# Kernel optimization log

Measured on AMD Instinct MI355X. Metric: run time of the kernel, lower is better.

Reference implementation:

```python
import jax, jax.numpy as jnp
import numpy as np

D_MODEL = 1024
NHEAD = 16
HEAD_DIM = D_MODEL // NHEAD
EPS = 1e-8


def setup_inputs() -> dict:
    key = jax.random.key(0)
    ks = jax.random.split(key, 10)
    B, T = 2, 2048
    s = 1.0 / np.sqrt(D_MODEL)
    return {
        "query": jax.random.normal(ks[0], (B, T, D_MODEL), jnp.float32),
        "key": jax.random.normal(ks[1], (B, T, D_MODEL), jnp.float32),
        "value": jax.random.normal(ks[2], (B, T, D_MODEL), jnp.float32),
        "frac": jax.random.uniform(ks[3], (B, T), jnp.float32),
        "Wq": jax.random.normal(ks[4], (D_MODEL, D_MODEL), jnp.float32) * s,
        "bq": jnp.zeros((D_MODEL,), jnp.float32),
        "Wk": jax.random.normal(ks[5], (D_MODEL, D_MODEL), jnp.float32) * s,
        "bk": jnp.zeros((D_MODEL,), jnp.float32),
        "Wv": jax.random.normal(ks[6], (D_MODEL, D_MODEL), jnp.float32) * s,
        "bv": jnp.zeros((D_MODEL,), jnp.float32),
        "attn_bias": jax.random.normal(ks[7], (HEAD_DIM,), jnp.float32) * 0.02,
        "Wo": jax.random.normal(ks[8], (D_MODEL, D_MODEL), jnp.float32) * s,
        "bo": jnpp if False else jnp.zeros((D_MODEL,), jnp.float32),
    }


def reference(query, key, value, frac, Wq, bq, Wk, bk, Wv, bv, attn_bias, Wo, bo):
    B, T, _ = query.shape
    H, Dh = NHEAD, HEAD_DIM
    scale = Dh ** -0.5

    # torch Linear: x @ W.T + b
    Q = (query @ Wq.T + bq).reshape(B, T, H, Dh).transpose(0, 2, 1, 3)  # [B,H,T,Dh]
    K = (key @ Wk.T + bk).reshape(B, T, H, Dh).transpose(0, 2, 1, 3)
    V = (value @ Wv.T + bv).reshape(B, T, H, Dh).transpose(0, 2, 1, 3)

    # factor_ij = (frac_j - frac_i) / (frac_i*frac_j + eps), shape [B,T,T]
    fi = frac[:, :, None]
    fj = frac[:, None, :]
    factor = (fj - fi) / (fi * fj + EPS)

    # sum_d (Q_i*K_j + attn_bias*factor)_d == QK^T + sum(attn_bias)*factor
    bias_sum = jnp.sum(attn_bias)
    logits = jnp.einsum('bhid,bhjd->bhij', Q, K) + bias_sum * factor[:, None, :, :]
    logits = logits * scale

    probs = jax.nn.softmax(logits, axis=-1)  # dropout p=0.0 (eval)
    out = jnp.einsum('bhij,bhjd->bhid', probs, V)  # [B,H,T,Dh]
    out = out.transpose(0, 2, 1, 3).reshape(B, T, H * Dh)
    return out @ Wo.T + bo
```

## Files before the change

### kernel.cpp

```cpp
#include <hip/hip_runtime.h>

typedef short s16x8 __attribute__((ext_vector_type(8)));
typedef float f32x4 __attribute__((ext_vector_type(4)));
typedef float f32x16 __attribute__((ext_vector_type(16)));
typedef unsigned int u32x2 __attribute__((ext_vector_type(2)));
typedef unsigned int u32x4 __attribute__((ext_vector_type(4)));
typedef unsigned short u16;
typedef unsigned int u32;

#define D_MODEL 1024
#define NHEAD   16
#define HD      64
#define TSEQ    2048
#define NB      2
#define MROWS   4096
#define NSPLIT  2
#define NTILES  (TSEQ / 64 / NSPLIT)

#define LOG2E 1.4426950408889634f
#define QSCALE (0.125f * LOG2E)

__device__ __forceinline__ u16 f2bf(float f) {
  unsigned u = __builtin_bit_cast(unsigned, f);
  u += 0x7fffu + ((u >> 16) & 1u);
  return (u16)(u >> 16);
}

__device__ __forceinline__ float bf2f(u16 x) {
  return __builtin_bit_cast(float, (u32)x << 16);
}

__device__ __forceinline__ u32 cvtpk(float lo, float hi) {
  u32 r;
  asm("v_cvt_pk_bf16_f32 %0, %1, %2" : "=v"(r) : "v"(lo), "v"(hi));
  return r;
}

__device__ __forceinline__ float exp2fast(float x) {
#if __has_builtin(__builtin_amdgcn_exp2f)
  return __builtin_amdgcn_exp2f(x);
#else
  return exp2f(x);
#endif
}

__device__ __forceinline__ float rcpfast(float x) {
#if __has_builtin(__builtin_amdgcn_rcpf)
  return __builtin_amdgcn_rcpf(x);
#else
  return 1.f / x;
#endif
}

__device__ __forceinline__ void gload16(const void* g, void* l) {
  __builtin_amdgcn_global_load_lds((const __attribute__((address_space(1))) void*)g,
                                   (__attribute__((address_space(3))) void*)l,
                                   16, 0, 0);
}

__global__ void cvt_all(const float* __restrict__ q, const float* __restrict__ k,
                        const float* __restrict__ v, const float* __restrict__ wq,
                        const float* __restrict__ wk, const float* __restrict__ wv,
                        const float* __restrict__ wo, const float* __restrict__ ab,
                        u16* qb, u16* kb, u16* vb, u16* wqb, u16* wkb, u16* wvb, u16* wob,
                        float* bsum) {
  if (blockIdx.x == 16384) {
    if (threadIdx.x < 64) {
      float s = ab[threadIdx.x];
#pragma unroll
      for (int m = 32; m >= 1; m >>= 1) s += __shfl_xor(s, m);
      if (threadIdx.x == 0) bsum[0] = s * 0.125f * LOG2E;
    }
    return;
  }
  int i = blockIdx.x * 256 + threadIdx.x;
  const float* src; u16* dst; int off;
  if (i < 3 * 1048576) {
    int t = i >> 20; off = i & 1048575;
    src = (t == 0) ? q : (t == 1) ? k : v;
    dst = (t == 0) ? qb : (t == 1) ? kb : vb;
  } else {
    int j = i - 3 * 1048576;
    int t = j >> 18; off = j & 262143;
    src = (t == 0) ? wq : (t == 1) ? wk : (t == 2) ? wv : wo;
    dst = (t == 0) ? wqb : (t == 1) ? wkb : (t == 2) ? wvb : wob;
  }
  float4 x = ((const float4*)src)[off];
  ushort4 o;
  o.x = f2bf(x.x); o.y = f2bf(x.y); o.z = f2bf(x.z); o.w = f2bf(x.w);
  ((ushort4*)dst)[off] = o;
}

template <int BM, int BN, int WN, int MODE>
__device__ __forceinline__ void gemm_core(const u16* __restrict__ A, const u16* __restrict__ Bt,
                                          const float* __restrict__ bias, void* __restrict__ out,
                                          float oscale, u16* lds) {
  constexpr int K = 1024, N = 1024;
  constexpr int WM = 4 / WN;
  constexpr int WTM = BM / WM, WTN = BN / WN;
  constexpr int MR = WTM / 16, NR = WTN / 16;
  constexpr int ASZ = BM * 32, BSZ = BN * 32;
  constexpr int AISS = ASZ / 2048, BISS = BSZ / 2048;
  u16* lA = lds;
  u16* lB = lds + 2 * ASZ;

  const int tid = threadIdx.x;
  const int wid = tid >> 6, lane = tid & 63;
  const int l15 = lane & 15, lgp = lane >> 4;
  const int wr = wid / WN, wc = wid % WN;
  const int m0 = blockIdx.y * BM, n0 = blockIdx.x * BN;

  const u16* gA[AISS];
  const u16* gB[BISS];
#pragma unroll
  for (int i = 0; i < AISS; ++i) {
    int tp = i * 256 + tid, row = tp % BM, kc = tp / BM;
    gA[i] = A + (size_t)(m0 + row) * K + kc * 8;
  }
#pragma unroll
  for (int i = 0; i < BISS; ++i) {
    int tp = i * 256 + tid, row = tp % BN, kc = tp / BN;
    gB[i] = Bt + (size_t)(n0 + row) * K + kc * 8;
  }

  f32x4 acc[MR][NR];
#pragma unroll
  for (int m = 0; m < MR; ++m)
#pragma unroll
    for (int n = 0; n < NR; ++n) acc[m][n] = (f32x4){0.f, 0.f, 0.f, 0.f};

  auto stage = [&](int buf, int k0) {
#pragma unroll
    for (int i = 0; i < AISS; ++i)
      gload16(gA[i] + k0, lA + buf * ASZ + (i * 256 + tid) * 8);
#pragma unroll
    for (int i = 0; i < BISS; ++i)
      gload16(gB[i] + k0, lB + buf * BSZ + (i * 256 + tid) * 8);
  };

  int cur = 0;
  stage(0, 0);
  __syncthreads();
  for (int k0 = 0; k0 < K; k0 += 32) {
    if (k0 + 32 < K) stage(cur ^ 1, k0 + 32);
    const u16* a = lA + cur * ASZ;
    const u16* b = lB + cur * BSZ;
    s16x8 af[MR], bf[NR];
#pragma unroll
    for (int m = 0; m < MR; ++m)
      af[m] = *(const s16x8*)(a + lgp * BM * 8 + (wr * WTM + m * 16 + l15) * 8);
#pragma unroll
    for (int n = 0; n < NR; ++n)
      bf[n] = *(const s16x8*)(b + lgp * BN * 8 + (wc * WTN + n * 16 + l15) * 8);
    __builtin_amdgcn_s_setprio(1);
#pragma unroll
    for (int m = 0; m < MR; ++m)
#pragma unroll
      for (int n = 0; n < NR; ++n) {
        if (MODE == 1)
          acc[m][n] = __builtin_amdgcn_mfma_f32_16x16x32_bf16(bf[n], af[m], acc[m][n], 0, 0, 0);
        else
          acc[m][n] = __builtin_amdgcn_mfma_f32_16x16x32_bf16(af[m], bf[n], acc[m][n], 0, 0, 0);
      }
    __builtin_amdgcn_s_setprio(0);
    __syncthreads();
    cur ^= 1;
  }

  if (MODE == 1) {
    float4 bvv4[NR];
#pragma unroll
    for (int n = 0; n < NR; ++n)
      bvv4[n] = *(const float4*)(bias + n0 + wc * WTN + n * 16 + lgp * 4);
#pragma unroll
    for (int m = 0; m < MR; ++m) {
      int m_abs = m0 + wr * WTM + m * 16 + l15;
      int bb = m_abs >> 11, t = m_abs & 2047;
#pragma unroll
      for (int n = 0; n < NR; ++n) {
#pragma unroll
        for (int r = 0; r < 4; ++r) {
          int n_abs = n0 + wc * WTN + n * 16 + lgp * 4 + r;
          int h = n_abs >> 6, d = n_abs & 63;
          float vv = (acc[m][n][r] + ((const float*)&bvv4[n])[r]) * oscale;
          ((u16*)out)[(((size_t)((bb * NHEAD + h) * HD + d)) << 11) + t] = f2bf(vv);
        }
      }
    }
  } else {
    float bvv[NR];
#pragma unroll
    for (int n = 0; n < NR; ++n) bvv[n] = bias[n0 + wc * WTN + n * 16 + l15];
#pragma unroll
    for (int m = 0; m < MR; ++m) {
      int rowb = m0 + wr * WTM + m * 16 + lgp * 4;
#pragma unroll
      for (int n = 0; n < NR; ++n) {
        int col = n0 + wc * WTN + n * 16 + l15;
#pragma unroll
        for (int r = 0; r < 4; ++r) {
          int row = rowb + r;
          float vv = (acc[m][n][r] + bvv[n]) * oscale;
          if (MODE == 2) {
            ((float*)out)[(size_t)row * N + col] = vv;
          } else {
            int b = row >> 11, t = row & 2047;
            int h = col >> 6, d = col & 63;
            ((u16*)out)[(((size_t)(b * NHEAD + h) * TSEQ + t) << 6) + d] = f2bf(vv);
          }
        }
      }
    }
  }
}

__global__ __launch_bounds__(256) void gemm_qkv(const u16* __restrict__ qb, const u16* __restrict__ kb,
                                                const u16* __restrict__ vb,
                                                const u16* __restrict__ Wqb, const u16* __restrict__ Wkb,
                                                const u16* __restrict__ Wvb,
                                                const float* __restrict__ bq, const float* __restrict__ bk,
                                                const float* __restrict__ bv,
                                                u16* Qp, u16* Kp, u16* Vtp) {
  __shared__ __align__(16) u16 lds[2 * 128 * 32 * 2];
  int z = blockIdx.z;
  if (z == 0)
    gemm_core<128, 128, 2, 0>(qb, Wqb, bq, Qp, QSCALE, lds);
  else if (z == 1)
    gemm_core<128, 128, 2, 0>(kb, Wkb, bk, Kp, 1.0f, lds);
  else
    gemm_core<128, 128, 2, 1>(vb, Wvb, bv, Vtp, 1.0f, lds);
}

__global__ __launch_bounds__(256) void gemm_out(const u16* __restrict__ A, const u16* __restrict__ Bt,
                                                const float* __restrict__ bias, float* __restrict__ out) {
  __shared__ __align__(16) u16 lds[2 * 64 * 32 + 2 * 128 * 32];
  gemm_core<64, 128, 4, 2>(A, Bt, bias, out, 1.0f, lds);
}

__global__ __launch_bounds__(256, 4) void attn_kernel(const u16* __restrict__ Qp,
                                                      const u16* __restrict__ Kp,
                                                      const u16* __restrict__ Vt,
                                                      const float* __restrict__ frac,
                                                      const float* __restrict__ bsum,
                                                      u16* __restrict__ o0,
                                                      u16* __restrict__ o1,
                                                      float2* __restrict__ ml) {
  __shared__ __align__(16) u16 kbuf[64 * 64];
  __shared__ __align__(16) u16 vbuf[2][64 * 64];
  const int tid = threadIdx.x, wid = tid >> 6, lane = tid & 63;
  const int l31 = lane & 31, hi = lane >> 5, hi4 = hi * 4, hi8 = hi * 8;
  const int ksw = l31 & 7;
  const int bh = blockIdx.y, b = bh >> 4, h = bh & 15;
  const int z = blockIdx.z;
  const int kvbase = z * (TSEQ / NSPLIT);
  u16* opart = z ? o1 : o0;
  float2* mlz = ml + z * (NB * NHEAD * TSEQ);
  const u16* Qh = Qp + (size_t)bh * TSEQ * HD;
  const u16* Kh = Kp + (size_t)bh * TSEQ * HD;
  const u16* Vh = Vt + (size_t)bh * HD * TSEQ;
  const float* fb = frac + b * TSEQ;
  const float bs = bsum[0];
  const float THR2 = 24.0f;
  const int q0w = blockIdx.x * 128 + wid * 32;

  const int r_0 = tid >> 3, c_0 = ((tid & 7) ^ (r_0 & 7)) * 8;
  const int r_1 = 32 + r_0, c_1 = ((tid & 7) ^ (r_1 & 7)) * 8;
  const u16* Ksrc0 = Kh + (size_t)r_0 * HD + c_0;
  const u16* Ksrc1 = Kh + (size_t)r_1 * HD + c_1;
  const u16* Vsrc0 = Vh + (size_t)r_0 * TSEQ + c_0;
  const u16* Vsrc1 = Vh + (size_t)r_1 * TSEQ + c_1;
  u16* kdst0 = &kbuf[(wid * 64) * 8];
  u16* kdst1 = &kbuf[(256 + wid * 64) * 8];

  s16x8 qf[4];
#pragma unroll
  for (int dc = 0; dc < 4; ++dc)
    qf[dc] = *(const s16x8*)(Qh + (size_t)(q0w + l31) * HD + dc * 16 + hi8);

  const float fi = fb[q0w + l31];
  const float nbfi = -bs * fi;
  float m2run = -1e30f, lsum = 0.f;
  f32x16 o2[2];
#pragma unroll
  for (int dh = 0; dh < 2; ++dh)
#pragma unroll
    for (int i = 0; i < 16; ++i) o2[dh][i] = 0.f;

  auto stage = [&](int buf, int t) {
    int kv0s = kvbase + t * 64;
    gload16(Ksrc0 + (size_t)kv0s * HD, kdst0);
    gload16(Ksrc1 + (size_t)kv0s * HD, kdst1);
    gload16(Vsrc0 + kv0s, &vbuf[buf][(wid * 64) * 8]);
    gload16(Vsrc1 + kv0s, &vbuf[buf][(256 + wid * 64) * 8]);
  };

  int cur = 0;
  stage(0, 0);
  __syncthreads();

  for (int t = 0; t < NTILES; ++t) {
    const int kvt = kvbase + t * 64;

    f32x16 s2[2];
    __builtin_amdgcn_s_setprio(1);
#pragma unroll
    for (int t2 = 0; t2 < 2; ++t2) {
      f32x16 a;
#pragma unroll
      for (int i = 0; i < 16; ++i) a[i] = 0.f;
#pragma unroll
      for (int dc = 0; dc < 4; ++dc) {
        s16x8 kf = *(const s16x8*)(&kbuf[(t2 * 32 + l31) * 64 + (((dc * 2 + hi) ^ ksw) * 8)]);
        a = __builtin_amdgcn_mfma_f32_32x32x16_bf16(kf, qf[dc], a, 0, 0, 0);
      }
      s2[t2] = a;
    }
    __builtin_amdgcn_s_setprio(0);

    __syncthreads();
    if (t + 1 < NTILES) stage(cur ^ 1, t + 1);

    float pmax = -1e30f;
#pragma unroll
    for (int t2 = 0; t2 < 2; ++t2) {
#pragma unroll
      for (int g = 0; g < 4; ++g) {
        float4 fj4 = *(const float4*)(fb + kvt + t2 * 32 + g * 8 + hi4);
#pragma unroll
        for (int r4 = 0; r4 < 4; ++r4) {
          float fjv = (r4 == 0) ? fj4.x : (r4 == 1) ? fj4.y : (r4 == 2) ? fj4.z : fj4.w;
          float num = __builtin_fmaf(bs, fjv, nbfi);
          float den = __builtin_fmaf(fi, fjv, 1e-8f);
          float l2 = __builtin_fmaf(num, rcpfast(den), s2[t2][g * 4 + r4]);
          s2[t2][g * 4 + r4] = l2;
          pmax = fmaxf(pmax, l2);
        }
      }
    }

    if (__any((pmax - m2run) > THR2)) {
      float tm = fmaxf(pmax, __shfl_xor(pmax, 32));
      float m2n = fmaxf(m2run, tm);
      float alpha = exp2fast(m2run - m2n);
      lsum *= alpha;
      m2run = m2n;
#pragma unroll
      for (int reg = 0; reg < 16; ++reg) {
        float av = __shfl(alpha, (reg & 3) + 8 * (reg >> 2) + hi4);
        o2[0][reg] *= av;
        o2[1][reg] *= av;
      }
    }

    s16x8 pa[4];
#pragma unroll
    for (int t2 = 0; t2 < 2; ++t2) {
      u32 uu[8];
#pragma unroll
      for (int k = 0; k < 8; ++k) {
        float p0 = exp2fast(s2[t2][2 * k + 0] - m2run);
        float p1 = exp2fast(s2[t2][2 * k + 1] - m2run);
        lsum += p0 + p1;
        uu[k] = cvtpk(p0, p1);
      }
      u32 a0 = uu[0], b0 = uu[2];
      asm("v_permlane32_swap_b32 %0, %1" : "+v"(a0), "+v"(b0));
      u32 a1 = uu[1], b1 = uu[3];
      asm("v_permlane32_swap_b32 %0, %1" : "+v"(a1), "+v"(b1));
      pa[t2 * 2] = __builtin_bit_cast(s16x8, (u32x4){a0, a1, b0, b1});
      u32 a2 = uu[4], b2 = uu[6];
      asm("v_permlane32_swap_b32 %0, %1" : "+v"(a2), "+v"(b2));
      u32 a3 = uu[5], b3 = uu[7];
      asm("v_permlane32_swap_b32 %0, %1" : "+v"(a3), "+v"(b3));
      pa[t2 * 2 + 1] = __builtin_bit_cast(s16x8, (u32x4){a2, a3, b2, b3});
    }

    const u16* vbp = &vbuf[cur][0];
    __builtin_amdgcn_s_setprio(1);
#pragma unroll
    for (int dh = 0; dh < 2; ++dh) {
#pragma unroll
      for (int ks = 0; ks < 4; ++ks) {
        s16x8 vf = *(const s16x8*)(vbp + (dh * 32 + l31) * 64 + (((ks * 2 + hi) ^ ksw) * 8));
        o2[dh] = __builtin_amdgcn_mfma_f32_32x32x16_bf16(pa[ks], vf, o2[dh], 0, 0, 0);
      }
    }
    __builtin_amdgcn_s_setprio(0);

    __syncthreads();
    cur ^= 1;
  }

  lsum += __shfl_xor(lsum, 32);
  if (hi == 0)
    mlz[(bh << 11) + q0w + l31] = make_float2(m2run, lsum);
#pragma unroll
  for (int dh = 0; dh < 2; ++dh)
#pragma unroll
    for (int reg = 0; reg < 16; ++reg) {
      int q = q0w + (reg & 3) + 8 * (reg >> 2) + hi4;
      opart[((size_t)(b * TSEQ + q)) * D_MODEL + h * HD + dh * 32 + l31] = f2bf(o2[dh][reg]);
    }
}

__global__ __launch_bounds__(256) void attn_combine(const u16* __restrict__ o0,
                                                    const u16* __restrict__ o1,
                                                    const float2* __restrict__ ml,
                                                    u16* __restrict__ aout) {
  int g = blockIdx.x * 256 + threadIdx.x;
  int bth = g >> 3, j0 = (g & 7) * 8;
  int b = bth >> 15, t = (bth >> 4) & 2047, h = bth & 15;
  int mlidx = (((b << 4) | h) << 11) | t;
  float2 v0 = ml[mlidx];
  float2 v1 = ml[NB * NHEAD * TSEQ + mlidx];
  float M = fmaxf(v0.x, v1.x);
  float a0 = exp2fast(v0.x - M), a1 = exp2fast(v1.x - M);
  float rd = __fdividef(1.f, __builtin_fmaf(v0.y, a0, v1.y * a1));
  float s0 = a0 * rd, s1 = a1 * rd;
  size_t base = (size_t)bth * 64 + j0;
  s16x8 x0 = *(const s16x8*)(o0 + base);
  s16x8 x1 = *(const s16x8*)(o1 + base);
  s16x8 out;
#pragma unroll
  for (int j = 0; j < 8; ++j) {
    float f = __builtin_fmaf(bf2f((u16)x0[j]), s0, bf2f((u16)x1[j]) * s1);
    out[j] = (short)f2bf(f);
  }
  *(s16x8*)(aout + base) = out;
}

extern "C" void kernel_launch(void* const* d_in, const int* in_sizes, int n_in,
                              void* d_out, int out_size, void* d_ws, size_t ws_size,
                              hipStream_t stream) {
  const float* query = (const float*)d_in[0];
  const float* key_  = (const float*)d_in[1];
  const float* value = (const float*)d_in[2];
  const float* frac  = (const float*)d_in[3];
  const float* Wq    = (const float*)d_in[4];
  const float* bq    = (const float*)d_in[5];
  const float* Wk    = (const float*)d_in[6];
  const float* bk    = (const float*)d_in[7];
  const float* Wv    = (const float*)d_in[8];
  const float* bv    = (const float*)d_in[9];
  const float* abias = (const float*)d_in[10];
  const float* Wo    = (const float*)d_in[11];
  const float* bo    = (const float*)d_in[12];

  char* ws = (char*)d_ws;
  size_t off = 0;
  auto alloc = [&](size_t bytes) { char* p = ws + off; off += (bytes + 255) & ~255ULL; return p; };
  const size_t XB = (size_t)MROWS * D_MODEL * 2;
  const size_t WB = (size_t)D_MODEL * D_MODEL * 2;
  u16* qb  = (u16*)alloc(XB);
  u16* kb  = (u16*)alloc(XB);
  u16* vb  = (u16*)alloc(XB);
  u16* Wqb = (u16*)alloc(WB);
  u16* Wkb = (u16*)alloc(WB);
  u16* Wvb = (u16*)alloc(WB);
  u16* Wob = (u16*)alloc(WB);
  float* bsum = (float*)alloc(256);
  u16* Qp  = (u16*)alloc(XB);
  u16* Kp  = (u16*)alloc(XB);
  u16* Vtp = (u16*)alloc(XB);
  u16* AO  = (u16*)alloc(XB);

  u16* o0 = qb;
  u16* o1 = kb;
  float2* ml = (float2*)vb;

  cvt_all<<<dim3(16385), dim3(256), 0, stream>>>(query, key_, value, Wq, Wk, Wv, Wo, abias,
                                                 qb, kb, vb, Wqb, Wkb, Wvb, Wob, bsum);

  gemm_qkv<<<dim3(D_MODEL / 128, MROWS / 128, 3), dim3(256), 0, stream>>>(
      qb, kb, vb, Wqb, Wkb, Wvb, bq, bk, bv, Qp, Kp, Vtp);

  attn_kernel<<<dim3(TSEQ / 128, NB * NHEAD, NSPLIT), dim3(256), 0, stream>>>(
      Qp, Kp, Vtp, frac, bsum, o0, o1, ml);

  attn_combine<<<dim3(MROWS * D_MODEL / 8 / 256), dim3(256), 0, stream>>>(o0, o1, ml, AO);

  gemm_out<<<dim3(D_MODEL / 128, MROWS / 64), dim3(256), 0, stream>>>(AO, Wob, bo, (float*)d_out);
}
```

Before: 181.7 us.

## Software-pipeline attention: overlap next-tile QK with current softmax and PV

Double-buffers the K tile in shared memory and restructures the attention loop into a two-stage pipeline. The QK^T MFMAs for tile t+1 are issued before the softmax and PV of tile t, and K and V loads are staged separately to hide latency. This costs more registers (two score accumulators), so the launch-bounds occupancy hint drops from 4 to 3. The ml buffer also gets its own workspace allocation instead of aliasing vb.

Measured after the change: 273.8 us. 50.7% more time.

```diff
diff --git a/kernel.cpp b/kernel.cpp
--- a/kernel.cpp
+++ b/kernel.cpp
@@ -15,7 +15,6 @@
 #define NB      2
 #define MROWS   4096
 #define NSPLIT  2
-#define NTILES  (TSEQ / 64 / NSPLIT)
 
 #define LOG2E 1.4426950408889634f
 #define QSCALE (0.125f * LOG2E)
@@ -237,7 +236,7 @@
   gemm_core<64, 128, 4, 2>(A, Bt, bias, out, 1.0f, lds);
 }
 
-__global__ __launch_bounds__(256, 4) void attn_kernel(const u16* __restrict__ Qp,
+__global__ __launch_bounds__(256, 3) void attn_kernel(const u16* __restrict__ Qp,
                                                       const u16* __restrict__ Kp,
                                                       const u16* __restrict__ Vt,
                                                       const float* __restrict__ frac,
@@ -245,7 +244,7 @@
                                                       u16* __restrict__ o0,
                                                       u16* __restrict__ o1,
                                                       float2* __restrict__ ml) {
-  __shared__ __align__(16) u16 kbuf[64 * 64];
+  __shared__ __align__(16) u16 kbuf[2][64 * 64];
   __shared__ __align__(16) u16 vbuf[2][64 * 64];
   const int tid = threadIdx.x, wid = tid >> 6, lane = tid & 63;
   const int l31 = lane & 31, hi = lane >> 5, hi4 = hi * 4, hi8 = hi * 8;
@@ -269,8 +268,6 @@
   const u16* Ksrc1 = Kh + (size_t)r_1 * HD + c_1;
   const u16* Vsrc0 = Vh + (size_t)r_0 * TSEQ + c_0;
   const u16* Vsrc1 = Vh + (size_t)r_1 * TSEQ + c_1;
-  u16* kdst0 = &kbuf[(wid * 64) * 8];
-  u16* kdst1 = &kbuf[(256 + wid * 64) * 8];
 
   s16x8 qf[4];
 #pragma unroll
@@ -286,22 +283,19 @@
 #pragma unroll
     for (int i = 0; i < 16; ++i) o2[dh][i] = 0.f;
 
-  auto stage = [&](int buf, int t) {
+  auto stageK = [&](int buf, int t) {
     int kv0s = kvbase + t * 64;
-    gload16(Ksrc0 + (size_t)kv0s * HD, kdst0);
-    gload16(Ksrc1 + (size_t)kv0s * HD, kdst1);
+    gload16(Ksrc0 + (size_t)kv0s * HD, &kbuf[buf][(wid * 64) * 8]);
+    gload16(Ksrc1 + (size_t)kv0s * HD, &kbuf[buf][(256 + wid * 64) * 8]);
+  };
+  auto stageV = [&](int buf, int t) {
+    int kv0s = kvbase + t * 64;
     gload16(Vsrc0 + kv0s, &vbuf[buf][(wid * 64) * 8]);
     gload16(Vsrc1 + kv0s, &vbuf[buf][(256 + wid * 64) * 8]);
   };
 
-  int cur = 0;
-  stage(0, 0);
-  __syncthreads();
-
-  for (int t = 0; t < NTILES; ++t) {
-    const int kvt = kvbase + t * 64;
-
-    f32x16 s2[2];
+  auto qk_phase = [&](f32x16 (&dst)[2], int kbi) {
+    const u16* kbp = &kbuf[kbi][0];
     __builtin_amdgcn_s_setprio(1);
 #pragma unroll
     for (int t2 = 0; t2 < 2; ++t2) {
@@ -310,16 +304,16 @@
       for (int i = 0; i < 16; ++i) a[i] = 0.f;
 #pragma unroll
       for (int dc = 0; dc < 4; ++dc) {
-        s16x8 kf = *(const s16x8*)(&kbuf[(t2 * 32 + l31) * 64 + (((dc * 2 + hi) ^ ksw) * 8)]);
+        s16x8 kf = *(const s16x8*)(kbp + (t2 * 32 + l31) * 64 + (((dc * 2 + hi) ^ ksw) * 8));
         a = __builtin_amdgcn_mfma_f32_32x32x16_bf16(kf, qf[dc], a, 0, 0, 0);
       }
-      s2[t2] = a;
+      dst[t2] = a;
     }
     __builtin_amdgcn_s_setprio(0);
-
-    __syncthreads();
-    if (t + 1 < NTILES) stage(cur ^ 1, t + 1);
-
+  };
+
+  auto sm_phase = [&](f32x16 (&s2)[2], int t, s16x8 (&pa)[4]) {
+    const int kvt = kvbase + t * 64;
     float pmax = -1e30f;
 #pragma unroll
     for (int t2 = 0; t2 < 2; ++t2) {
@@ -337,7 +331,6 @@
         }
       }
     }
-
     if (__any((pmax - m2run) > THR2)) {
       float tm = fmaxf(pmax, __shfl_xor(pmax, 32));
       float m2n = fmaxf(m2run, tm);
@@ -351,8 +344,6 @@
         o2[1][reg] *= av;
       }
     }
-
-    s16x8 pa[4];
 #pragma unroll
     for (int t2 = 0; t2 < 2; ++t2) {
       u32 uu[8];
@@ -374,8 +365,10 @@
       asm("v_permlane32_swap_b32 %0, %1" : "+v"(a3), "+v"(b3));
       pa[t2 * 2 + 1] = __builtin_bit_cast(s16x8, (u32x4){a2, a3, b2, b3});
     }
-
-    const u16* vbp = &vbuf[cur][0];
+  };
+
+  auto pv_phase = [&](int vbi, s16x8 (&pa)[4]) {
+    const u16* vbp = &vbuf[vbi][0];
     __builtin_amdgcn_s_setprio(1);
 #pragma unroll
     for (int dh = 0; dh < 2; ++dh) {
@@ -386,9 +379,38 @@
       }
     }
     __builtin_amdgcn_s_setprio(0);
-
-    __syncthreads();
-    cur ^= 1;
+  };
+
+  f32x16 s2a[2], s2b[2];
+
+  stageK(0, 0); stageV(0, 0);
+  stageK(1, 1); stageV(1, 1);
+  __syncthreads();
+  qk_phase(s2a, 0);
+  __syncthreads();
+
+  for (int p = 0; p < 8; ++p) {
+    const bool more = (p < 7);
+    {
+      const int t0 = 2 * p;
+      if (more) stageK(0, t0 + 2);
+      qk_phase(s2b, 1);
+      s16x8 pa[4];
+      sm_phase(s2a, t0, pa);
+      pv_phase(0, pa);
+      __syncthreads();
+      if (more) stageV(0, t0 + 2);
+    }
+    {
+      const int t1 = 2 * p + 1;
+      if (more) stageK(1, t1 + 2);
+      if (more) qk_phase(s2a, 0);
+      s16x8 pa[4];
+      sm_phase(s2b, t1, pa);
+      pv_phase(1, pa);
+      __syncthreads();
+      if (more) stageV(1, t1 + 2);
+    }
   }
 
   lsum += __shfl_xor(lsum, 32);
@@ -463,10 +485,10 @@
   u16* Kp  = (u16*)alloc(XB);
   u16* Vtp = (u16*)alloc(XB);
   u16* AO  = (u16*)alloc(XB);
+  float2* ml = (float2*)alloc((size_t)NSPLIT * NB * NHEAD * TSEQ * sizeof(float2));
 
   u16* o0 = qb;
   u16* o1 = kb;
-  float2* ml = (float2*)vb;
 
   cvt_all<<<dim3(16385), dim3(256), 0, stream>>>(query, key_, value, Wq, Wk, Wv, Wo, abias,
                                                  qb, kb, vb, Wqb, Wkb, Wvb, Wob, bsum);
```

## Fuse fp32-to-bf16 activation conversion into QKV GEMM A-tile loads

Applied to the files above, without the earlier changes.

Removes the separate conversion pass over query/key/value and has the QKV GEMM read fp32 activations directly. It loads them into registers a stage ahead, converts with packed bf16 instructions and writes them to LDS, while weights still use async global-to-LDS loads. This avoids writing and re-reading three 8MB bf16 activation copies. In exchange each GEMM tile reads twice the A bytes from global memory and adds register pressure and conversion work inside the main loop.

Result: slower. 212.6 us (+17.0%).

```diff
diff --git a/kernel.cpp b/kernel.cpp
--- a/kernel.cpp
+++ b/kernel.cpp
@@ -15,7 +15,6 @@
 #define NB      2
 #define MROWS   4096
 #define NSPLIT  2
-#define NTILES  (TSEQ / 64 / NSPLIT)
 
 #define LOG2E 1.4426950408889634f
 #define QSCALE (0.125f * LOG2E)
@@ -58,13 +57,11 @@
                                    16, 0, 0);
 }
 
-__global__ void cvt_all(const float* __restrict__ q, const float* __restrict__ k,
-                        const float* __restrict__ v, const float* __restrict__ wq,
-                        const float* __restrict__ wk, const float* __restrict__ wv,
-                        const float* __restrict__ wo, const float* __restrict__ ab,
-                        u16* qb, u16* kb, u16* vb, u16* wqb, u16* wkb, u16* wvb, u16* wob,
-                        float* bsum) {
-  if (blockIdx.x == 16384) {
+__global__ void cvt_w(const float* __restrict__ wq, const float* __restrict__ wk,
+                      const float* __restrict__ wv, const float* __restrict__ wo,
+                      const float* __restrict__ ab,
+                      u16* wqb, u16* wkb, u16* wvb, u16* wob, float* bsum) {
+  if (blockIdx.x == 4096) {
     if (threadIdx.x < 64) {
       float s = ab[threadIdx.x];
 #pragma unroll
@@ -74,17 +71,9 @@
     return;
   }
   int i = blockIdx.x * 256 + threadIdx.x;
-  const float* src; u16* dst; int off;
-  if (i < 3 * 1048576) {
-    int t = i >> 20; off = i & 1048575;
-    src = (t == 0) ? q : (t == 1) ? k : v;
-    dst = (t == 0) ? qb : (t == 1) ? kb : vb;
-  } else {
-    int j = i - 3 * 1048576;
-    int t = j >> 18; off = j & 262143;
-    src = (t == 0) ? wq : (t == 1) ? wk : (t == 2) ? wv : wo;
-    dst = (t == 0) ? wqb : (t == 1) ? wkb : (t == 2) ? wvb : wob;
-  }
+  int t = i >> 18, off = i & 262143;
+  const float* src = (t == 0) ? wq : (t == 1) ? wk : (t == 2) ? wv : wo;
+  u16* dst = (t == 0) ? wqb : (t == 1) ? wkb : (t == 2) ? wvb : wob;
   float4 x = ((const float4*)src)[off];
   ushort4 o;
   o.x = f2bf(x.x); o.y = f2bf(x.y); o.z = f2bf(x.z); o.w = f2bf(x.w);
@@ -92,9 +81,145 @@
 }
 
 template <int BM, int BN, int WN, int MODE>
+__device__ __forceinline__ void gemm_core_f32A(const float* __restrict__ Af,
+                                               const u16* __restrict__ Bt,
+                                               const float* __restrict__ bias,
+                                               void* __restrict__ out,
+                                               float oscale, u16* lds) {
+  constexpr int K = 1024, N = 1024;
+  constexpr int WM = 4 / WN;
+  constexpr int WTM = BM / WM, WTN = BN / WN;
+  constexpr int MR = WTM / 16, NR = WTN / 16;
+  constexpr int ASZ = BM * 32, BSZ = BN * 32;
+  constexpr int BISS = BSZ / 2048;
+  u16* lA = lds;
+  u16* lB = lds + 2 * ASZ;
+
+  const int tid = threadIdx.x;
+  const int wid = tid >> 6, lane = tid & 63;
+  const int l15 = lane & 15, lgp = lane >> 4;
+  const int wr = wid / WN, wc = wid % WN;
+  const int m0 = blockIdx.y * BM, n0 = blockIdx.x * BN;
+
+  const int rowA = tid % BM;
+  const int kcA0 = tid / BM, kcA1 = kcA0 + 256 / BM;
+  const float* gAf = Af + (size_t)(m0 + rowA) * K;
+
+  const u16* gB[BISS];
+#pragma unroll
+  for (int i = 0; i < BISS; ++i) {
+    int tp = i * 256 + tid, row = tp % BN, kc = tp / BN;
+    gB[i] = Bt + (size_t)(n0 + row) * K + kc * 8;
+  }
+
+  f32x4 acc[MR][NR];
+#pragma unroll
+  for (int m = 0; m < MR; ++m)
+#pragma unroll
+    for (int n = 0; n < NR; ++n) acc[m][n] = (f32x4){0.f, 0.f, 0.f, 0.f};
+
+  auto stageB = [&](int buf, int k0) {
+#pragma unroll
+    for (int i = 0; i < BISS; ++i)
+      gload16(gB[i] + k0, lB + buf * BSZ + (i * 256 + tid) * 8);
+  };
+  float4 rA[4];
+  auto loadA = [&](int k0) {
+    const float4* s0 = (const float4*)(gAf + k0 + kcA0 * 8);
+    rA[0] = s0[0]; rA[1] = s0[1];
+    const float4* s1 = (const float4*)(gAf + k0 + kcA1 * 8);
+    rA[2] = s1[0]; rA[3] = s1[1];
+  };
+  auto writeA = [&](int buf) {
+    u32x4 w0 = (u32x4){cvtpk(rA[0].x, rA[0].y), cvtpk(rA[0].z, rA[0].w),
+                       cvtpk(rA[1].x, rA[1].y), cvtpk(rA[1].z, rA[1].w)};
+    *(u32x4*)(lA + buf * ASZ + (size_t)tid * 8) = w0;
+    u32x4 w1 = (u32x4){cvtpk(rA[2].x, rA[2].y), cvtpk(rA[2].z, rA[2].w),
+                       cvtpk(rA[3].x, rA[3].y), cvtpk(rA[3].z, rA[3].w)};
+    *(u32x4*)(lA + buf * ASZ + (size_t)(256 + tid) * 8) = w1;
+  };
+
+  loadA(0);
+  stageB(0, 0);
+  writeA(0);
+  loadA(32);
+  __syncthreads();
+
+  int cur = 0;
+  for (int k0 = 0; k0 < K; k0 += 32) {
+    if (k0 + 32 < K) { writeA(cur ^ 1); stageB(cur ^ 1, k0 + 32); }
+    if (k0 + 64 < K) loadA(k0 + 64);
+    const u16* a = lA + cur * ASZ;
+    const u16* b = lB + cur * BSZ;
+    s16x8 af[MR], bf[NR];
+#pragma unroll
+    for (int m = 0; m < MR; ++m)
+      af[m] = *(const s16x8*)(a + lgp * BM * 8 + (wr * WTM + m * 16 + l15) * 8);
+#pragma unroll
+    for (int n = 0; n < NR; ++n)
+      bf[n] = *(const s16x8*)(b + lgp * BN * 8 + (wc * WTN + n * 16 + l15) * 8);
+    __builtin_amdgcn_s_setprio(1);
+#pragma unroll
+    for (int m = 0; m < MR; ++m)
+#pragma unroll
+      for (int n = 0; n < NR; ++n) {
+        if (MODE == 1)
+          acc[m][n] = __builtin_amdgcn_mfma_f32_16x16x32_bf16(bf[n], af[m], acc[m][n], 0, 0, 0);
+        else
+          acc[m][n] = __builtin_amdgcn_mfma_f32_16x16x32_bf16(af[m], bf[n], acc[m][n], 0, 0, 0);
+      }
+    __builtin_amdgcn_s_setprio(0);
+    __syncthreads();
+    cur ^= 1;
+  }
+
+  if (MODE == 1) {
+    float4 bvv4[NR];
+#pragma unroll
+    for (int n = 0; n < NR; ++n)
+      bvv4[n] = *(const float4*)(bias + n0 + wc * WTN + n * 16 + lgp * 4);
+#pragma unroll
+    for (int m = 0; m < MR; ++m) {
+      int m_abs = m0 + wr * WTM + m * 16 + l15;
+      int bb = m_abs >> 11, t = m_abs & 2047;
+#pragma unroll
+      for (int n = 0; n < NR; ++n) {
+#pragma unroll
+        for (int r = 0; r < 4; ++r) {
+          int n_abs = n0 + wc * WTN + n * 16 + lgp * 4 + r;
+          int h = n_abs >> 6, d = n_abs & 63;
+          float vv = (acc[m][n][r] + ((const float*)&bvv4[n])[r]) * oscale;
+          ((u16*)out)[(((size_t)((bb * NHEAD + h) * HD + d)) << 11) + t] = f2bf(vv);
+        }
+      }
+    }
+  } else {
+    float bvv[NR];
+#pragma unroll
+    for (int n = 0; n < NR; ++n) bvv[n] = bias[n0 + wc * WTN + n * 16 + l15];
+#pragma unroll
+    for (int m = 0; m < MR; ++m) {
+      int rowb = m0 + wr * WTM + m * 16 + lgp * 4;
+#pragma unroll
+      for (int n = 0; n < NR; ++n) {
+        int col = n0 + wc * WTN + n * 16 + l15;
+#pragma unroll
+        for (int r = 0; r < 4; ++r) {
+          int row = rowb + r;
+          float vv = (acc[m][n][r] + bvv[n]) * oscale;
+          int b = row >> 11, t = row & 2047;
+          int h = col >> 6, d = col & 63;
+          ((u16*)out)[(((size_t)(b * NHEAD + h) * TSEQ + t) << 6) + d] = f2bf(vv);
+        }
+      }
+    }
+  }
+}
+
+template <int BM, int BN, int WN>
 __device__ __forceinline__ void gemm_core(const u16* __restrict__ A, const u16* __restrict__ Bt,
-                                          const float* __restrict__ bias, void* __restrict__ out,
-                                          float oscale, u16* lds) {
+                                          const float* __restrict__ bias, float* __restrict__ out,
+                                          u16* lds) {
   constexpr int K = 1024, N = 1024;
   constexpr int WM = 4 / WN;
   constexpr int WTM = BM / WM, WTN = BN / WN;
@@ -156,66 +281,32 @@
 #pragma unroll
     for (int m = 0; m < MR; ++m)
 #pragma unroll
-      for (int n = 0; n < NR; ++n) {
-        if (MODE == 1)
-          acc[m][n] = __builtin_amdgcn_mfma_f32_16x16x32_bf16(bf[n], af[m], acc[m][n], 0, 0, 0);
-        else
-          acc[m][n] = __builtin_amdgcn_mfma_f32_16x16x32_bf16(af[m], bf[n], acc[m][n], 0, 0, 0);
-      }
+      for (int n = 0; n < NR; ++n)
+        acc[m][n] = __builtin_amdgcn_mfma_f32_16x16x32_bf16(af[m], bf[n], acc[m][n], 0, 0, 0);
     __builtin_amdgcn_s_setprio(0);
     __syncthreads();
     cur ^= 1;
   }
 
-  if (MODE == 1) {
-    float4 bvv4[NR];
-#pragma unroll
-    for (int n = 0; n < NR; ++n)
-      bvv4[n] = *(const float4*)(bias + n0 + wc * WTN + n * 16 + lgp * 4);
-#pragma unroll
-    for (int m = 0; m < MR; ++m) {
-      int m_abs = m0 + wr * WTM + m * 16 + l15;
-      int bb = m_abs >> 11, t = m_abs & 2047;
-#pragma unroll
-      for (int n = 0; n < NR; ++n) {
-#pragma unroll
-        for (int r = 0; r < 4; ++r) {
-          int n_abs = n0 + wc * WTN + n * 16 + lgp * 4 + r;
-          int h = n_abs >> 6, d = n_abs & 63;
-          float vv = (acc[m][n][r] + ((const float*)&bvv4[n])[r]) * oscale;
-          ((u16*)out)[(((size_t)((bb * NHEAD + h) * HD + d)) << 11) + t] = f2bf(vv);
-        }
-      }
-    }
-  } else {
-    float bvv[NR];
-#pragma unroll
-    for (int n = 0; n < NR; ++n) bvv[n] = bias[n0 + wc * WTN + n * 16 + l15];
-#pragma unroll
-    for (int m = 0; m < MR; ++m) {
-      int rowb = m0 + wr * WTM + m * 16 + lgp * 4;
-#pragma unroll
-      for (int n = 0; n < NR; ++n) {
-        int col = n0 + wc * WTN + n * 16 + l15;
-#pragma unroll
-        for (int r = 0; r < 4; ++r) {
-          int row = rowb + r;
-          float vv = (acc[m][n][r] + bvv[n]) * oscale;
-          if (MODE == 2) {
-            ((float*)out)[(size_t)row * N + col] = vv;
-          } else {
-            int b = row >> 11, t = row & 2047;
-            int h = col >> 6, d = col & 63;
-            ((u16*)out)[(((size_t)(b * NHEAD + h) * TSEQ + t) << 6) + d] = f2bf(vv);
-          }
-        }
-      }
-    }
-  }
-}
-
-__global__ __launch_bounds__(256) void gemm_qkv(const u16* __restrict__ qb, const u16* __restrict__ kb,
-                                                const u16* __restrict__ vb,
+  float bvv[NR];
+#pragma unroll
+  for (int n = 0; n < NR; ++n) bvv[n] = bias[n0 + wc * WTN + n * 16 + l15];
+#pragma unroll
+  for (int m = 0; m < MR; ++m) {
+    int rowb = m0 + wr * WTM + m * 16 + lgp * 4;
+#pragma unroll
+    for (int n = 0; n < NR; ++n) {
+      int col = n0 + wc * WTN + n * 16 + l15;
+#pragma unroll
+      for (int r = 0; r < 4; ++r)
+        out[(size_t)(rowb + r) * N + col] = acc[m][n][r] + bvv[n];
+    }
+  }
+}
+
+__global__ __launch_bounds__(256) void gemm_qkv(const float* __restrict__ query,
+                                                const float* __restrict__ key_,
+                                                const float* __restrict__ value,
                                                 const u16* __restrict__ Wqb, const u16* __restrict__ Wkb,
                                                 const u16* __restrict__ Wvb,
                                                 const float* __restrict__ bq, const float* __restrict__ bk,
@@ -224,17 +315,17 @@
   __shared__ __align__(16) u16 lds[2 * 128 * 32 * 2];
   int z = blockIdx.z;
   if (z == 0)
-    gemm_core<128, 128, 2, 0>(qb, Wqb, bq, Qp, QSCALE, lds);
+    gemm_core_f32A<128, 128, 2, 0>(query, Wqb, bq, Qp, QSCALE, lds);
   else if (z == 1)
-    gemm_core<128, 128, 2, 0>(kb, Wkb, bk, Kp, 1.0f, lds);
+    gemm_core_f32A<128, 128, 2, 0>(key_, Wkb, bk, Kp, 1.0f, lds);
   else
-    gemm_core<128, 128, 2, 1>(vb, Wvb, bv, Vtp, 1.0f, lds);
+    gemm_core_f32A<128, 128, 2, 1>(value, Wvb, bv, Vtp, 1.0f, lds);
 }
 
 __global__ __launch_bounds__(256) void gemm_out(const u16* __restrict__ A, const u16* __restrict__ Bt,
                                                 const float* __restrict__ bias, float* __restrict__ out) {
   __shared__ __align__(16) u16 lds[2 * 64 * 32 + 2 * 128 * 32];
-  gemm_core<64, 128, 4, 2>(A, Bt, bias, out, 1.0f, lds);
+  gemm_core<64, 128, 4>(A, Bt, bias, out, lds);
 }
 
 __global__ __launch_bounds__(256, 4) void attn_kernel(const u16* __restrict__ Qp,
@@ -253,6 +344,7 @@
   const int bh = blockIdx.y, b = bh >> 4, h = bh & 15;
   const int z = blockIdx.z;
   const int kvbase = z * (TSEQ / NSPLIT);
+  const int NT = TSEQ / 64 / NSPLIT;
   u16* opart = z ? o1 : o0;
   float2* mlz = ml + z * (NB * NHEAD * TSEQ);
   const u16* Qh = Qp + (size_t)bh * TSEQ * HD;
@@ -298,7 +390,7 @@
   stage(0, 0);
   __syncthreads();
 
-  for (int t = 0; t < NTILES; ++t) {
+  for (int t = 0; t < NT; ++t) {
     const int kvt = kvbase + t * 64;
 
     f32x16 s2[2];
@@ -318,7 +410,7 @@
     __builtin_amdgcn_s_setprio(0);
 
     __syncthreads();
-    if (t + 1 < NTILES) stage(cur ^ 1, t + 1);
+    if (t + 1 < NT) stage(cur ^ 1, t + 1);
 
     float pmax = -1e30f;
 #pragma unroll
@@ -451,9 +543,6 @@
   auto alloc = [&](size_t bytes) { char* p = ws + off; off += (bytes + 255) & ~255ULL; return p; };
   const size_t XB = (size_t)MROWS * D_MODEL * 2;
   const size_t WB = (size_t)D_MODEL * D_MODEL * 2;
-  u16* qb  = (u16*)alloc(XB);
-  u16* kb  = (u16*)alloc(XB);
-  u16* vb  = (u16*)alloc(XB);
   u16* Wqb = (u16*)alloc(WB);
   u16* Wkb = (u16*)alloc(WB);
   u16* Wvb = (u16*)alloc(WB);
@@ -463,16 +552,15 @@
   u16* Kp  = (u16*)alloc(XB);
   u16* Vtp = (u16*)alloc(XB);
   u16* AO  = (u16*)alloc(XB);
-
-  u16* o0 = qb;
-  u16* o1 = kb;
-  float2* ml = (float2*)vb;
-
-  cvt_all<<<dim3(16385), dim3(256), 0, stream>>>(query, key_, value, Wq, Wk, Wv, Wo, abias,
-                                                 qb, kb, vb, Wqb, Wkb, Wvb, Wob, bsum);
+  u16* o0  = (u16*)alloc(XB);
+  u16* o1  = (u16*)alloc(XB);
+  float2* ml = (float2*)alloc((size_t)NSPLIT * NB * NHEAD * TSEQ * sizeof(float2));
+
+  cvt_w<<<dim3(4097), dim3(256), 0, stream>>>(Wq, Wk, Wv, Wo, abias,
+                                              Wqb, Wkb, Wvb, Wob, bsum);
 
   gemm_qkv<<<dim3(D_MODEL / 128, MROWS / 128, 3), dim3(256), 0, stream>>>(
-      qb, kb, vb, Wqb, Wkb, Wvb, bq, bk, bv, Qp, Kp, Vtp);
+      query, key_, value, Wqb, Wkb, Wvb, bq, bk, bv, Qp, Kp, Vtp);
 
   attn_kernel<<<dim3(TSEQ / 128, NB * NHEAD, NSPLIT), dim3(256), 0, stream>>>(
       Qp, Kp, Vtp, frac, bsum, o0, o1, ml);
```
